# Kernel tuning notes

Measured on AMD Instinct MI355X. Metric: run time of the kernel, lower is better.

Reference implementation:

```python
import jax, jax.numpy as jnp
import numpy as np
import math

D_SINGLE, D_PAIR, H, PQ, PV = 384, 128, 12, 4, 8
DH = D_SINGLE // H
OUT_DIM = H * DH + H * PV * 4 + H * D_PAIR


def setup_inputs() -> dict:
    key = jax.random.key(0)
    ks = jax.random.split(key, 24)
    B, L = 1, 512
    inp = {
        'single': jax.random.normal(ks[0], (B, L, D_SINGLE), jnp.float32),
        'pair': jax.random.normal(ks[1], (B, L, L, D_PAIR), jnp.float32),
        'rot_mats': jax.random.normal(ks[2], (B, L, 3, 3), jnp.float32),
        'trans': jax.random.normal(ks[3], (B, L, 3), jnp.float32),
        'mask': jnp.ones((B, L), jnp.float32),
        'ln_w': jnp.ones((D_SINGLE,), jnp.float32),
        'ln_b': jnp.zeros((D_SINGLE,), jnp.float32),
        'Wq': jax.random.normal(ks[4], (D_SINGLE, H * DH), jnp.float32) * 0.02,
        'bq': jnp.zeros((H * DH,), jnp.float32),
        'Wk': jax.random.normal(ks[5], (D_SINGLE, H * DH), jnp.float32) * 0.02,
        'bk': jnp.zeros((H * DH,), jnp.float32),
        'Wv': jax.random.normal(ks[6], (D_SINGLE, H * DH), jnp.float32) * 0.02,
        'bv': jnp.zeros((H * DH,), jnp.float32),
        'Wqp': jax.random.normal(ks[7], (D_SINGLE, H * PQ * 3), jnp.float32) * 0.02,
        'bqp': jnp.zeros((H * PQ * 3,), jnp.float32),
        'Wkp': jax.random.normal(ks[8], (D_SINGLE, H * PQ * 3), jnp.float32) * 0.02,
        'bkp': jnp.zeros((H * PQ * 3,), jnp.float32),
        'Wvp': jax.random.normal(ks[9], (D_SINGLE, H * PV * 3), jnp.float32) * 0.02,
        'bvp': jnp.zeros((H * PV * 3,), jnp.float32),
        'Wpb': jax.random.normal(ks[10], (D_PAIR, H), jnp.float32) * 0.02,
        'bpb': jnp.zeros((H,), jnp.float32),
        'Wo': jax.random.normal(ks[11], (OUT_DIM, D_SINGLE), jnp.float32) * 0.02,
        'bo': jnp.zeros((D_SINGLE,), jnp.float32),
        'w_c': jnp.asarray(1.0 / math.sqrt(3.0), jnp.float32),
        'w_l': jnp.asarray(1.0 / 3.0, jnp.float32),
        'gamma_h': jnp.ones((H,), jnp.float32),
    }
    return inp


def _layer_norm(x, w, b, eps=1e-5):
    mu = jnp.mean(x, axis=-1, keepdims=True)
    var = jnp.mean((x - mu) ** 2, axis=-1, keepdims=True)
    return (x - mu) * jax.lax.rsqrt(var + eps) * w + b


def reference(single, pair, rot_mats, trans, mask, ln_w, ln_b, Wq, bq, Wk, bk, Wv, bv,
              Wqp, bqp, Wkp, bkp, Wvp, bvp, Wpb, bpb, Wo, bo, w_c, w_l, gamma_h):
    B, L, _ = single.shape
    sn = _layer_norm(single, ln_w, ln_b)
    q = (sn @ Wq + bq).reshape(B, L, H, DH)
    k = (sn @ Wk + bk).reshape(B, L, H, DH)
    v = (sn @ Wv + bv).reshape(B, L, H, DH)
    qp = (sn @ Wqp + bqp).reshape(B, L, H, PQ, 3)
    kp = (sn @ Wkp + bkp).reshape(B, L, H, PQ, 3)
    vp = (sn @ Wvp + bvp).reshape(B, L, H, PV, 3)

    t = trans[:, :, None, None, :]  # [B,L,1,1,3]
    qg = jnp.einsum('blij,blhpj->blhpi', rot_mats, qp) + t
    kg = jnp.einsum('blij,blhpj->blhpi', rot_mats, kp) + t
    vg = jnp.einsum('blij,blhpj->blhpi', rot_mats, vp) + t

    # sequence logits [B,H,L,L]
    seq_logits = jnp.einsum('bihd,bjhd->bhij', q, k) * w_c / math.sqrt(DH)

    # geometric logits: pairwise point distances [B,H,L,L]
    q_pts = jnp.transpose(qg, (0, 2, 1, 3, 4))  # [B,H,L,PQ,3]
    k_pts = jnp.transpose(kg, (0, 2, 1, 3, 4))
    diff = q_pts[:, :, :, None] - k_pts[:, :, None]  # [B,H,L,L,PQ,3]
    dist_sq = jnp.sum(diff ** 2, axis=-1)            # [B,H,L,L,PQ]
    geo_logits = -0.5 * jnp.sum(dist_sq, axis=-1) * gamma_h[None, :, None, None] * w_l

    pair_bias = jnp.transpose(pair @ Wpb + bpb, (0, 3, 1, 2))  # [B,H,L,L]
    logits = seq_logits + geo_logits + pair_bias

    mask_2d = (mask[:, :, None] * mask[:, None, :])[:, None]  # [B,1,L,L]
    logits = jnp.where(mask_2d > 0, logits, jnp.float32(-1e9))
    attn = jax.nn.softmax(logits, axis=-1)  # [B,H,L,L]

    # sequence aggregation -> [B,L,H,DH]
    seq_out = jnp.einsum('bhij,bjhd->bihd', attn, v).reshape(B, L, H * DH)

    # point aggregation -> local frame features
    pts_out = jnp.einsum('bhij,bjhpd->bihpd', attn, vg)  # [B,L,H,PV,3]
    pts_local = jnp.einsum('blji,blhpj->blhpi', rot_mats, pts_out - t)
    pts_norm = jnp.linalg.norm(pts_local, axis=-1, keepdims=True)
    pts_feat = jnp.concatenate([pts_norm, pts_local], axis=-1).reshape(B, L, H * PV * 4)

    # pair aggregation -> [B,L,H*D_PAIR]
    pair_out = jnp.einsum('bhij,bijd->bihd', attn, pair).reshape(B, L, H * D_PAIR)

    combined = jnp.concatenate([seq_out, pts_feat, pair_out], axis=-1)
    return combined @ Wo + bo
```

## Files before the change

### kernel.cpp

```cpp
#include <hip/hip_runtime.h>
#include <math.h>

#define LQ    512
#define DS    384
#define DPAIR 128
#define NH    12
#define NPP   1792
#define FE    48
#define TJC   64
#define NC    8

typedef unsigned short u16;
typedef unsigned int   u32;
typedef __attribute__((ext_vector_type(8))) short bf16x8;
typedef __attribute__((ext_vector_type(4))) float f32x4;

__device__ inline u16 bf16_rne(float x) {
  u32 u = __float_as_uint(x);
  u32 r = (u + 0x7FFFu + ((u >> 16) & 1u)) >> 16;
  return (u16)r;
}
__device__ inline void split_bf16(float x, u16& h, u16& l) {
  u16 hb = bf16_rne(x);
  float hf = __uint_as_float(((u32)hb) << 16);
  h = hb;
  l = bf16_rne(x - hf);
}

__global__ __launch_bounds__(256) void k_concat_wT(
    const float* __restrict__ Wq, const float* __restrict__ Wk,
    const float* __restrict__ Wv, const float* __restrict__ Wqp,
    const float* __restrict__ Wkp, const float* __restrict__ Wvp,
    const float* __restrict__ bq, const float* __restrict__ bk,
    const float* __restrict__ bv, const float* __restrict__ bqp,
    const float* __restrict__ bkp, const float* __restrict__ bvp,
    const float* __restrict__ Wpb,
    u16* __restrict__ Wth, u16* __restrict__ Wtl,
    float* __restrict__ bcat, float* __restrict__ WpbT) {
  int blk = blockIdx.x, t = threadIdx.x;
  if (blk < 168) {
    __shared__ u16 hi[64][66], lo[64][66];
    int kb = blk / 28, cb = blk % 28;
    int k0 = kb * 64, c0 = cb * 64;
    for (int e = t; e < 4096; e += 256) {
      int rr = e >> 6, cc = e & 63;
      int k = k0 + rr, c = c0 + cc;
      float v = 0.f;
      if (c < 384)       v = Wq[k*384 + c];
      else if (c < 768)  v = Wk[k*384 + c-384];
      else if (c < 1152) v = Wv[k*384 + c-768];
      else if (c < 1296) v = Wqp[k*144 + c-1152];
      else if (c < 1440) v = Wkp[k*144 + c-1296];
      else if (c < 1728) v = Wvp[k*288 + c-1440];
      u16 h_, l_; split_bf16(v, h_, l_);
      hi[rr][cc] = h_; lo[rr][cc] = l_;
    }
    __syncthreads();
    for (int e = t; e < 4096; e += 256) {
      int cc = e >> 6, kk = e & 63;
      Wth[(size_t)(c0+cc)*DS + k0 + kk] = hi[kk][cc];
      Wtl[(size_t)(c0+cc)*DS + k0 + kk] = lo[kk][cc];
    }
  } else {
    for (int e = t; e < NPP + NH*DPAIR; e += 256) {
      if (e < NPP) {
        int c = e;
        float v = 0.f;
        if (c < 384)       v = bq[c];
        else if (c < 768)  v = bk[c-384];
        else if (c < 1152) v = bv[c-768];
        else if (c < 1296) v = bqp[c-1152];
        else if (c < 1440) v = bkp[c-1296];
        else if (c < 1728) v = bvp[c-1440];
        bcat[c] = v;
      } else {
        int e2 = e - NPP;
        int k = e2 / NH, h = e2 % NH;
        WpbT[h*DPAIR + k] = Wpb[e2];
      }
    }
  }
}

__global__ __launch_bounds__(256) void k_transpose_split(
    const float* __restrict__ src, u16* __restrict__ dh, u16* __restrict__ dl,
    int R, int Cc) {
  __shared__ u16 hi[64][66], lo[64][66];
  int r0 = blockIdx.x * 64, c0 = blockIdx.y * 64, t = threadIdx.x;
  for (int e = t; e < 4096; e += 256) {
    int rr = e >> 6, cc = e & 63;
    float v = src[(size_t)(r0+rr)*Cc + c0 + cc];
    u16 h_, l_; split_bf16(v, h_, l_);
    hi[rr][cc] = h_; lo[rr][cc] = l_;
  }
  __syncthreads();
  for (int e = t; e < 4096; e += 256) {
    int cc = e >> 6, rr = e & 63;
    dh[(size_t)(c0+cc)*R + r0 + rr] = hi[rr][cc];
    dl[(size_t)(c0+cc)*R + r0 + rr] = lo[rr][cc];
  }
}

__global__ void k_split4(const float* __restrict__ src, u16* __restrict__ h,
                         u16* __restrict__ l, int n4) {
  int e = blockIdx.x * 256 + threadIdx.x;
  if (e >= n4) return;
  float4 v = ((const float4*)src)[e];
  u16 h0,l0,h1,l1,h2,l2,h3,l3;
  split_bf16(v.x, h0, l0); split_bf16(v.y, h1, l1);
  split_bf16(v.z, h2, l2); split_bf16(v.w, h3, l3);
  uint2 hp, lp;
  hp.x = (u32)h0 | ((u32)h1 << 16); hp.y = (u32)h2 | ((u32)h3 << 16);
  lp.x = (u32)l0 | ((u32)l1 << 16); lp.y = (u32)l2 | ((u32)l3 << 16);
  ((uint2*)h)[e] = hp; ((uint2*)l)[e] = lp;
}

__global__ __launch_bounds__(128) void k_layernorm(const float* __restrict__ x,
                                                   const float* __restrict__ w,
                                                   const float* __restrict__ b,
                                                   u16* __restrict__ yh,
                                                   u16* __restrict__ yl) {
  __shared__ float red[128];
  __shared__ float s_mu, s_rstd;
  int i = blockIdx.x, t = threadIdx.x;
  float v0 = x[i*DS + t], v1 = x[i*DS + t + 128], v2 = x[i*DS + t + 256];
  red[t] = v0 + v1 + v2; __syncthreads();
  for (int s = 64; s > 0; s >>= 1) { if (t < s) red[t] += red[t+s]; __syncthreads(); }
  if (t == 0) s_mu = red[0] * (1.f/384.f);
  __syncthreads();
  float mu = s_mu;
  float d0 = v0-mu, d1 = v1-mu, d2 = v2-mu;
  red[t] = d0*d0 + d1*d1 + d2*d2; __syncthreads();
  for (int s = 64; s > 0; s >>= 1) { if (t < s) red[t] += red[t+s]; __syncthreads(); }
  if (t == 0) s_rstd = rsqrtf(red[0] * (1.f/384.f) + 1e-5f);
  __syncthreads();
  float r = s_rstd;
  float y0 = d0*r*w[t      ] + b[t      ];
  float y1 = d1*r*w[t + 128] + b[t + 128];
  float y2 = d2*r*w[t + 256] + b[t + 256];
  u16 h_, l_;
  split_bf16(y0, h_, l_); yh[i*DS + t      ] = h_; yl[i*DS + t      ] = l_;
  split_bf16(y1, h_, l_); yh[i*DS + t + 128] = h_; yl[i*DS + t + 128] = l_;
  split_bf16(y2, h_, l_); yh[i*DS + t + 256] = h_; yl[i*DS + t + 256] = l_;
}

__global__ __launch_bounds__(256) void k_gemm_mfma(
    const u16* __restrict__ Ah, const u16* __restrict__ Al,
    const u16* __restrict__ Bth, const u16* __restrict__ Btl,
    const float* __restrict__ bias, float* __restrict__ C,
    float* __restrict__ Cpart, int M, int N, int K) {
  int t = threadIdx.x;
  int lane = t & 63, wave = t >> 6;
  int wr = wave >> 1, wc = wave & 1;
  int i0 = blockIdx.y * 64 + wr * 32;
  int j0 = blockIdx.x * 64 + wc * 32;
  int KS = gridDim.z;
  int kper = K / KS;
  size_t kbeg = (size_t)blockIdx.z * kper;
  int lr = lane & 15, lk = (lane >> 4) << 3;

  const u16* a0h = Ah  + (size_t)(i0 + lr) * K + kbeg + lk;
  const u16* a1h = a0h + (size_t)16 * K;
  const u16* a0l = Al  + (size_t)(i0 + lr) * K + kbeg + lk;
  const u16* a1l = a0l + (size_t)16 * K;
  const u16* b0h = Bth + (size_t)(j0 + lr) * K + kbeg + lk;
  const u16* b1h = b0h + (size_t)16 * K;
  const u16* b0l = Btl + (size_t)(j0 + lr) * K + kbeg + lk;
  const u16* b1l = b0l + (size_t)16 * K;

  f32x4 c00 = {0.f,0.f,0.f,0.f}, c01 = c00, c10 = c00, c11 = c00;
  for (int k = 0; k < kper; k += 32) {
    bf16x8 A0h = *(const bf16x8*)(a0h + k);
    bf16x8 A1h = *(const bf16x8*)(a1h + k);
    bf16x8 B0h = *(const bf16x8*)(b0h + k);
    bf16x8 B1h = *(const bf16x8*)(b1h + k);
    bf16x8 A0l = *(const bf16x8*)(a0l + k);
    bf16x8 A1l = *(const bf16x8*)(a1l + k);
    bf16x8 B0l = *(const bf16x8*)(b0l + k);
    bf16x8 B1l = *(const bf16x8*)(b1l + k);
    c00 = __builtin_amdgcn_mfma_f32_16x16x32_bf16(A0h, B0h, c00, 0, 0, 0);
    c01 = __builtin_amdgcn_mfma_f32_16x16x32_bf16(A0h, B1h, c01, 0, 0, 0);
    c10 = __builtin_amdgcn_mfma_f32_16x16x32_bf16(A1h, B0h, c10, 0, 0, 0);
    c11 = __builtin_amdgcn_mfma_f32_16x16x32_bf16(A1h, B1h, c11, 0, 0, 0);
    c00 = __builtin_amdgcn_mfma_f32_16x16x32_bf16(A0h, B0l, c00, 0, 0, 0);
    c01 = __builtin_amdgcn_mfma_f32_16x16x32_bf16(A0h, B1l, c01, 0, 0, 0);
    c10 = __builtin_amdgcn_mfma_f32_16x16x32_bf16(A1h, B0l, c10, 0, 0, 0);
    c11 = __builtin_amdgcn_mfma_f32_16x16x32_bf16(A1h, B1l, c11, 0, 0, 0);
    c00 = __builtin_amdgcn_mfma_f32_16x16x32_bf16(A0l, B0h, c00, 0, 0, 0);
    c01 = __builtin_amdgcn_mfma_f32_16x16x32_bf16(A0l, B1h, c01, 0, 0, 0);
    c10 = __builtin_amdgcn_mfma_f32_16x16x32_bf16(A1l, B0h, c10, 0, 0, 0);
    c11 = __builtin_amdgcn_mfma_f32_16x16x32_bf16(A1l, B1h, c11, 0, 0, 0);
  }

  int orow = (lane >> 4) << 2;
  int col0 = j0 + lr, col1 = j0 + 16 + lr;
  if (KS == 1) {
    float bb0 = bias[col0], bb1 = bias[col1];
    #pragma unroll
    for (int r = 0; r < 4; r++) {
      int row0 = i0 + orow + r, row1 = row0 + 16;
      C[(size_t)row0*N + col0] = c00[r] + bb0;
      C[(size_t)row0*N + col1] = c01[r] + bb1;
      C[(size_t)row1*N + col0] = c10[r] + bb0;
      C[(size_t)row1*N + col1] = c11[r] + bb1;
    }
  } else {
    float* dst = Cpart + (size_t)blockIdx.z * M * N;
    #pragma unroll
    for (int r = 0; r < 4; r++) {
      int row0 = i0 + orow + r, row1 = row0 + 16;
      dst[(size_t)row0*N + col0] = c00[r];
      dst[(size_t)row0*N + col1] = c01[r];
      dst[(size_t)row1*N + col0] = c10[r];
      dst[(size_t)row1*N + col1] = c11[r];
    }
  }
}

__global__ void k_reduce_bias(const float* __restrict__ part, const float* __restrict__ bias,
                              float* __restrict__ out, int MN, int N, int KS) {
  int e = blockIdx.x * 256 + threadIdx.x;
  if (e >= MN) return;
  float s = bias[e % N];
  for (int z = 0; z < KS; z++) s += part[(size_t)z*MN + e];
  out[e] = s;
}

__global__ void k_rotfeat(const float* __restrict__ C1, const float* __restrict__ rot,
                          const float* __restrict__ trans, const float* __restrict__ gamma,
                          const float* __restrict__ w_c, const float* __restrict__ w_l,
                          float* __restrict__ Af, float* __restrict__ Bf,
                          float* __restrict__ vgb) {
  int idx = blockIdx.x * 256 + threadIdx.x;
  if (idx >= LQ*NH) return;
  int h = idx % NH, i = idx / NH;
  float R[9], tr[3];
  #pragma unroll
  for (int r = 0; r < 9; r++) R[r] = rot[(size_t)i*9 + r];
  #pragma unroll
  for (int r = 0; r < 3; r++) tr[r] = trans[(size_t)i*3 + r];

  float s  = w_c[0] * rsqrtf(32.f);
  float gp = gamma[h] * w_l[0];
  float* a  = Af + ((size_t)h*LQ + i)*FE;
  float* bb = Bf + ((size_t)h*LQ + i)*FE;
  const float* q = C1 + (size_t)i*NPP + h*32;
  const float* k = C1 + (size_t)i*NPP + 384 + h*32;
  #pragma unroll 8
  for (int d = 0; d < 32; d++) { a[d] = s*q[d]; bb[d] = k[d]; }

  const float* qp = C1 + (size_t)i*NPP + 1152 + h*12;
  const float* kp = C1 + (size_t)i*NPP + 1296 + h*12;
  float sq = 0.f, sk = 0.f;
  #pragma unroll
  for (int p = 0; p < 4; p++) {
    float x = qp[p*3], y = qp[p*3+1], z = qp[p*3+2];
    #pragma unroll
    for (int r = 0; r < 3; r++) {
      float g = fmaf(R[r*3],x, fmaf(R[r*3+1],y, fmaf(R[r*3+2],z, tr[r])));
      a[32 + p*3 + r] = gp*g;
      sq = fmaf(g,g,sq);
    }
    float xk = kp[p*3], yk = kp[p*3+1], zk = kp[p*3+2];
    #pragma unroll
    for (int r = 0; r < 3; r++) {
      float g = fmaf(R[r*3],xk, fmaf(R[r*3+1],yk, fmaf(R[r*3+2],zk, tr[r])));
      bb[32 + p*3 + r] = g;
      sk = fmaf(g,g,sk);
    }
  }
  a[44] = -0.5f*gp*sq; a[45] = 1.f; a[46] = 0.f; a[47] = 0.f;
  bb[44] = 1.f; bb[45] = -0.5f*gp*sk; bb[46] = 0.f; bb[47] = 0.f;

  const float* vp = C1 + (size_t)i*NPP + 1440 + h*24;
  float* vd = vgb + ((size_t)i*NH + h)*24;
  #pragma unroll
  for (int p = 0; p < 8; p++) {
    float x = vp[p*3], y = vp[p*3+1], z = vp[p*3+2];
    #pragma unroll
    for (int r = 0; r < 3; r++)
      vd[p*3 + r] = fmaf(R[r*3],x, fmaf(R[r*3+1],y, fmaf(R[r*3+2],z, tr[r])));
  }
}

__global__ __launch_bounds__(256) void k_logits_nt(const float* __restrict__ Af,
                                                   const float* __restrict__ Bf,
                                                   float* __restrict__ S) {
  __shared__ float As[48*68];
  __shared__ float Bs[48*68];
  int h = blockIdx.z;
  int i0 = blockIdx.y * 64, j0 = blockIdx.x * 64;
  int t = threadIdx.x;
  int mg = t >> 4, ng = t & 15;
  const float* Ahp = Af + (size_t)h*LQ*FE;
  const float* Bhp = Bf + (size_t)h*LQ*FE;
  for (int e = t; e < 64*48; e += 256) {
    int m = e / 48, k = e % 48;
    As[k*68 + m] = Ahp[(size_t)(i0+m)*FE + k];
    Bs[k*68 + m] = Bhp[(size_t)(j0+m)*FE + k];
  }
  __syncthreads();
  float acc[4][4] = {};
  #pragma unroll 8
  for (int k = 0; k < 48; k++) {
    float4 av = *(const float4*)(As + k*68 + mg*4);
    float4 bv = *(const float4*)(Bs + k*68 + ng*4);
    float a[4] = {av.x, av.y, av.z, av.w};
    float b[4] = {bv.x, bv.y, bv.z, bv.w};
    #pragma unroll
    for (int y = 0; y < 4; y++)
      #pragma unroll
      for (int x = 0; x < 4; x++)
        acc[y][x] = fmaf(a[y], b[x], acc[y][x]);
  }
  #pragma unroll
  for (int y = 0; y < 4; y++) {
    #pragma unroll
    for (int x = 0; x < 4; x++)
      S[((size_t)h*LQ + i0 + mg*4 + y)*LQ + j0 + ng*4 + x] = acc[y][x];
  }
}

__global__ __launch_bounds__(256, 2) void k_pair_chunk(
    const float* __restrict__ pair, const float* __restrict__ WpbT,
    const float* __restrict__ bpb, const float* __restrict__ mask,
    float* __restrict__ S, float* __restrict__ pairpart, float* __restrict__ msum) {
  __shared__ float tile[TJC*133];
  __shared__ float wt[NH*TJC];
  int i = blockIdx.x, c = blockIdx.y, t = threadIdx.x;
  int j0 = c*TJC;

  const float4* src = (const float4*)(pair + ((size_t)i*LQ + j0)*DPAIR);
  #pragma unroll
  for (int u = 0; u < 8; u++) {
    int e = t + u*256; int row = e >> 5, c4 = e & 31;
    *(float4*)&tile[row*133 + c4*4] = src[e];
  }

  int j = t & 63;
  int hg = __builtin_amdgcn_readfirstlane(t >> 6);
  int h0 = hg*3;
  float l[3];
  #pragma unroll
  for (int q = 0; q < 3; q++)
    l[q] = S[((size_t)(h0+q)*LQ + i)*LQ + j0 + j] + bpb[h0+q];
  bool dead = (mask[i] * mask[j0 + j] <= 0.f);
  __syncthreads();

  {
    const float* w0p = WpbT + (size_t)(h0+0)*DPAIR;
    const float* w1p = WpbT + (size_t)(h0+1)*DPAIR;
    const float* w2p = WpbT + (size_t)(h0+2)*DPAIR;
    float a0 = 0.f, a1 = 0.f, a2 = 0.f;
    #pragma unroll 8
    for (int k = 0; k < DPAIR; k += 4) {
      float4 pv = *(const float4*)&tile[j*133 + k];
      float4 w0 = *(const float4*)(w0p + k);
      float4 w1 = *(const float4*)(w1p + k);
      float4 w2 = *(const float4*)(w2p + k);
      a0 = fmaf(pv.x,w0.x, fmaf(pv.y,w0.y, fmaf(pv.z,w0.z, fmaf(pv.w,w0.w, a0))));
      a1 = fmaf(pv.x,w1.x, fmaf(pv.y,w1.y, fmaf(pv.z,w1.z, fmaf(pv.w,w1.w, a1))));
      a2 = fmaf(pv.x,w2.x, fmaf(pv.y,w2.y, fmaf(pv.z,w2.z, fmaf(pv.w,w2.w, a2))));
    }
    l[0] += a0; l[1] += a1; l[2] += a2;
    if (dead) { l[0] = -1e9f; l[1] = -1e9f; l[2] = -1e9f; }
  }

  #pragma unroll
  for (int q = 0; q < 3; q++) {
    float m = l[q];
    #pragma unroll
    for (int o = 32; o > 0; o >>= 1) m = fmaxf(m, __shfl_xor(m, o, 64));
// ... 14 lines not shown
  float4 pv[8];
  #pragma unroll
  for (int q = 0; q < 8; q++) pv[q] = *(const float4*)&tile[(jb+q)*133 + dg*4];
  float4 acc[NH];
  #pragma unroll
  for (int h = 0; h < NH; h++) acc[h] = make_float4(0.f,0.f,0.f,0.f);
  #pragma unroll
  for (int h = 0; h < NH; h++) {
    float4 w0 = *(const float4*)&wt[h*TJC + jb];
    float4 w1 = *(const float4*)&wt[h*TJC + jb + 4];
    float wq[8] = {w0.x,w0.y,w0.z,w0.w,w1.x,w1.y,w1.z,w1.w};
    float4 a = acc[h];
    #pragma unroll
    for (int q = 0; q < 8; q++) {
      a.x = fmaf(wq[q], pv[q].x, a.x);
      a.y = fmaf(wq[q], pv[q].y, a.y);
      a.z = fmaf(wq[q], pv[q].z, a.z);
      a.w = fmaf(wq[q], pv[q].w, a.w);
    }
    acc[h] = a;
  }
  __syncthreads();

  float4* red4 = (float4*)tile;
  float4 tot[2];
  tot[0] = make_float4(0.f,0.f,0.f,0.f);
  tot[1] = make_float4(0.f,0.f,0.f,0.f);
  #pragma unroll
  for (int half = 0; half < 2; half++) {
    if ((strip >> 2) == half) {
      #pragma unroll
      for (int h = 0; h < NH; h++)
        red4[(((strip & 3)*NH) + h)*32 + dg] = acc[h];
    }
    __syncthreads();
    for (int e = t, u = 0; e < NH*32; e += 256, u++) {
      int rh = e >> 5, rd = e & 31;
      #pragma unroll
      for (int s4 = 0; s4 < 4; s4++) {
        float4 v = red4[((s4*NH) + rh)*32 + rd];
        tot[u].x += v.x; tot[u].y += v.y; tot[u].z += v.z; tot[u].w += v.w;
      }
    }
    __syncthreads();
  }
  for (int e = t, u = 0; e < NH*32; e += 256, u++) {
    int rh = e >> 5, rd = e & 31;
    *(float4*)&pairpart[(((size_t)i*NC + c)*NH + rh)*DPAIR + rd*4] = tot[u];
  }
}

__global__ __launch_bounds__(384) void k_scs_pairout(
    const float* __restrict__ msum, const float* __restrict__ pairpart,
    float* __restrict__ scs_g, float* __restrict__ comb) {
  __shared__ float scs[NH*NC];
  int i = blockIdx.x, t = threadIdx.x;
  if (t < NH) {
    float m = -3.0e38f;
    float mc[NC], sc_[NC];
    #pragma unroll
    for (int c = 0; c < NC; c++) {
      const float* p = msum + (((size_t)i*NC + c)*NH + t)*2;
      mc[c] = p[0]; sc_[c] = p[1];
      m = fmaxf(m, mc[c]);
    }
    float s = 0.f;
    #pragma unroll
    for (int c = 0; c < NC; c++) s += sc_[c] * __expf(mc[c] - m);
    float inv = 1.f / s;
    #pragma unroll
    for (int c = 0; c < NC; c++) {
      float v = __expf(mc[c] - m) * inv;
      scs[t*NC + c] = v;
      scs_g[((size_t)i*NH + t)*NC + c] = v;
    }
  }
  __syncthreads();
  int h = t >> 5, d = t & 31;
  float4 tot = make_float4(0.f,0.f,0.f,0.f);
  #pragma unroll
  for (int c = 0; c < NC; c++) {
    float sc = scs[h*NC + c];
    float4 v = *(const float4*)&pairpart[(((size_t)i*NC + c)*NH + h)*DPAIR + d*4];
    tot.x = fmaf(v.x, sc, tot.x); tot.y = fmaf(v.y, sc, tot.y);
    tot.z = fmaf(v.z, sc, tot.z); tot.w = fmaf(v.w, sc, tot.w);
  }
  *(float4*)&comb[(size_t)i*2304 + 768 + h*DPAIR + d*4] = tot;
}

__global__ __launch_bounds__(256) void k_attn_v(const float* __restrict__ attn,
                                                const float* __restrict__ C1,
                                                const float* __restrict__ vg,
                                                const float* __restrict__ scs,
                                                float* __restrict__ psum) {
  __shared__ float As[64*68];
  __shared__ float Vs[64*68];
  int i0 = blockIdx.x * 64;
  int h = blockIdx.y;
  int z = blockIdx.z;
  int t = threadIdx.x;
  int mg = t >> 4, ng = t & 15;
  float acc[4][4] = {};
  for (int k0 = z*128; k0 < z*128 + 128; k0 += 64) {
    int c = k0 >> 6;
    __syncthreads();
    for (int e = t; e < 64*64; e += 256) {
      int m = e >> 6, j = e & 63;
      float sc = scs[((size_t)(i0+m)*NH + h)*NC + c];
      As[j*68 + m] = attn[((size_t)h*LQ + i0 + m)*LQ + k0 + j] * sc;
    }
    for (int e = t; e < 64*64; e += 256) {
      int j = e >> 6, cc = e & 63;
      float v = 0.f;
      if (cc < 32)      v = C1[(size_t)(k0+j)*NPP + 768 + h*32 + cc];
      else if (cc < 56) v = vg[((size_t)(k0+j)*NH + h)*24 + (cc-32)];
      Vs[j*68 + cc] = v;
    }
    __syncthreads();
    #pragma unroll 4
    for (int j = 0; j < 64; j++) {
      float4 av = *(const float4*)(As + j*68 + mg*4);
      float4 bv = *(const float4*)(Vs + j*68 + ng*4);
      float a[4] = {av.x, av.y, av.z, av.w};
      float b[4] = {bv.x, bv.y, bv.z, bv.w};
      #pragma unroll
      for (int y = 0; y < 4; y++)
        #pragma unroll
        for (int x = 0; x < 4; x++)
          acc[y][x] = fmaf(a[y], b[x], acc[y][x]);
    }
  }
  #pragma unroll
  for (int y = 0; y < 4; y++) {
    int i = i0 + mg*4 + y;
    #pragma unroll
    for (int x = 0; x < 4; x++) {
      int n = ng*4 + x;
      psum[(((size_t)z*LQ + i)*NH + h)*64 + n] = acc[y][x];
    }
  }
}

__global__ void k_avpts(const float* __restrict__ psum, const float* __restrict__ rot,
                        const float* __restrict__ trans, float* __restrict__ comb) {
  int idx = blockIdx.x * 256 + threadIdx.x;
  if (idx >= LQ*NH*40) return;
  int w = idx % 40; int ih = idx / 40; int h = ih % NH; int i = ih / NH;
  size_t base = ((size_t)i*NH + h)*64;
  if (w < 32) {
    float s = 0.f;
    for (int z = 0; z < 4; z++) s += psum[(size_t)z*LQ*NH*64 + base + w];
    comb[(size_t)i*2304 + h*32 + w] = s;
  } else {
    int p = w - 32;
    float g[3];
    #pragma unroll
    for (int r = 0; r < 3; r++) {
      int n = 32 + p*3 + r;
      float s = 0.f;
      for (int z = 0; z < 4; z++) s += psum[(size_t)z*LQ*NH*64 + base + n];
      g[r] = s;
    }
    const float* R = rot + (size_t)i*9;
    const float* tr = trans + (size_t)i*3;
    float x = g[0]-tr[0], y = g[1]-tr[1], z = g[2]-tr[2];
    float lx = fmaf(R[0],x, fmaf(R[3],y, R[6]*z));
    float ly = fmaf(R[1],x, fmaf(R[4],y, R[7]*z));
    float lz = fmaf(R[2],x, fmaf(R[5],y, R[8]*z));
    float nrm = sqrtf(fmaf(lx,lx, fmaf(ly,ly, lz*lz)));
    float* dst = comb + (size_t)i*2304 + 384 + (h*8 + p)*4;
    dst[0] = nrm; dst[1] = lx; dst[2] = ly; dst[3] = lz;
  }
}

extern "C" void kernel_launch(void* const* d_in, const int* in_sizes, int n_in,
                              void* d_out, int out_size, void* d_ws, size_t ws_size,
                              hipStream_t stream) {
  const float* single = (const float*)d_in[0];
  const float* pair   = (const float*)d_in[1];
  const float* rot    = (const float*)d_in[2];
  const float* trans  = (const float*)d_in[3];
  const float* mask   = (const float*)d_in[4];
  const float* ln_w   = (const float*)d_in[5];
  const float* ln_b   = (const float*)d_in[6];
  const float* Wq     = (const float*)d_in[7];
  const float* bq     = (const float*)d_in[8];
  const float* Wk     = (const float*)d_in[9];
  const float* bk     = (const float*)d_in[10];
  const float* Wv     = (const float*)d_in[11];
  const float* bv     = (const float*)d_in[12];
  const float* Wqp    = (const float*)d_in[13];
  const float* bqp    = (const float*)d_in[14];
  const float* Wkp    = (const float*)d_in[15];
  const float* bkp    = (const float*)d_in[16];
  const float* Wvp    = (const float*)d_in[17];
  const float* bvp    = (const float*)d_in[18];
  const float* Wpb    = (const float*)d_in[19];
  const float* bpb    = (const float*)d_in[20];
  const float* Wo     = (const float*)d_in[21];
  const float* bo     = (const float*)d_in[22];
  const float* w_c    = (const float*)d_in[23];
  const float* w_l    = (const float*)d_in[24];
  const float* gamma  = (const float*)d_in[25];
  float* out = (float*)d_out;

  float* p = (float*)d_ws;
  auto alloc = [&](size_t n) { float* r = p; p += n; return r; };
  u16* WcatTh = (u16*)alloc((size_t)NPP*DS/2);
  u16* WcatTl = (u16*)alloc((size_t)NPP*DS/2);
  u16* snh    = (u16*)alloc((size_t)LQ*DS/2);
  u16* snl    = (u16*)alloc((size_t)LQ*DS/2);
  u16* WoTh   = (u16*)alloc((size_t)DS*2304/2);
  u16* WoTl   = (u16*)alloc((size_t)DS*2304/2);
  u16* combh  = (u16*)alloc((size_t)LQ*2304/2);
  u16* combl  = (u16*)alloc((size_t)LQ*2304/2);
  float* bcat    = alloc(NPP);
  float* WpbT    = alloc((size_t)NH*DPAIR);
  float* C1      = alloc((size_t)LQ*NPP);
  float* vgb     = alloc((size_t)LQ*NH*24);
  float* Af      = alloc((size_t)NH*LQ*FE);
  float* Bf      = alloc((size_t)NH*LQ*FE);
  float* S       = alloc((size_t)NH*LQ*LQ);
  float* pairpart= alloc((size_t)LQ*NC*NH*DPAIR);
  float* msum    = alloc((size_t)LQ*NC*NH*2);
  float* scs_g   = alloc((size_t)LQ*NH*NC);
  float* comb    = alloc((size_t)LQ*2304);
  float* scratch = alloc((size_t)2*LQ*NPP);

  k_concat_wT<<<dim3(169), 256, 0, stream>>>(
      Wq, Wk, Wv, Wqp, Wkp, Wvp, bq, bk, bv, bqp, bkp, bvp, Wpb,
      WcatTh, WcatTl, bcat, WpbT);
  k_transpose_split<<<dim3(2304/64, DS/64), 256, 0, stream>>>(Wo, WoTh, WoTl, 2304, DS);
  k_layernorm<<<dim3(LQ), 128, 0, stream>>>(single, ln_w, ln_b, snh, snl);
  k_gemm_mfma<<<dim3(NPP/64, LQ/64, 1), 256, 0, stream>>>(
      snh, snl, WcatTh, WcatTl, bcat, C1, nullptr, LQ, NPP, DS);
  k_rotfeat<<<dim3((LQ*NH + 255)/256), 256, 0, stream>>>(C1, rot, trans, gamma, w_c, w_l, Af, Bf, vgb);
  k_logits_nt<<<dim3(LQ/64, LQ/64, NH), 256, 0, stream>>>(Af, Bf, S);
  k_pair_chunk<<<dim3(LQ, NC), 256, 0, stream>>>(pair, WpbT, bpb, mask, S, pairpart, msum);
  k_scs_pairout<<<dim3(LQ), 384, 0, stream>>>(msum, pairpart, scs_g, comb);
  k_attn_v<<<dim3(LQ/64, NH, 4), 256, 0, stream>>>(S, C1, vgb, scs_g, scratch);
  k_avpts<<<dim3((LQ*NH*40 + 255)/256), 256, 0, stream>>>(scratch, rot, trans, comb);
  k_split4<<<dim3((LQ*2304/4 + 255)/256), 256, 0, stream>>>(comb, combh, combl, LQ*2304/4);
  k_gemm_mfma<<<dim3(DS/64, LQ/64, 8), 256, 0, stream>>>(
      combh, combl, WoTh, WoTl, nullptr, nullptr, scratch, LQ, DS, 2304);
  k_reduce_bias<<<dim3((LQ*DS + 255)/256), 256, 0, stream>>>(scratch, bo, out, LQ*DS, DS, 8);
}
```

Baseline: 384.2 us.

## Move logits and attention-value GEMMs to split-bf16 MFMA and fuse prep kernels

Replaces the scalar FP32 logits and attention-times-values GEMMs with split-bf16 MFMA kernels (hi/lo, three products), padding features to 64. The producers (rotfeat, scs_pairout, avpts) now emit bf16 hi/lo operands directly. This removes the separate split4 pass and the fp32 comb buffer. The weight-transpose, Wo-transpose and layernorm kernels are merged into one launch. In exchange it adds an extra pass that writes the scaled attention weights as two bf16 arrays, and rounding error from the split-bf16 approximation.

```diff
diff --git a/kernel.cpp b/kernel.cpp
--- a/kernel.cpp
+++ b/kernel.cpp
@@ -6,7 +6,7 @@
 #define DPAIR 128
 #define NH    12
 #define NPP   1792
-#define FE    48
+#define FE2   64
 #define TJC   64
 #define NC    8
 
@@ -27,19 +27,23 @@
   l = bf16_rne(x - hf);
 }
 
-__global__ __launch_bounds__(256) void k_concat_wT(
+__global__ __launch_bounds__(256) void k_prep(
     const float* __restrict__ Wq, const float* __restrict__ Wk,
     const float* __restrict__ Wv, const float* __restrict__ Wqp,
     const float* __restrict__ Wkp, const float* __restrict__ Wvp,
     const float* __restrict__ bq, const float* __restrict__ bk,
     const float* __restrict__ bv, const float* __restrict__ bqp,
     const float* __restrict__ bkp, const float* __restrict__ bvp,
-    const float* __restrict__ Wpb,
+    const float* __restrict__ Wpb, const float* __restrict__ Wo,
+    const float* __restrict__ xs, const float* __restrict__ ln_w,
+    const float* __restrict__ ln_b,
     u16* __restrict__ Wth, u16* __restrict__ Wtl,
-    float* __restrict__ bcat, float* __restrict__ WpbT) {
+    float* __restrict__ bcat, float* __restrict__ WpbT,
+    u16* __restrict__ WoTh, u16* __restrict__ WoTl,
+    u16* __restrict__ snh, u16* __restrict__ snl) {
+  __shared__ u16 sh_hi[64][66], sh_lo[64][66];
   int blk = blockIdx.x, t = threadIdx.x;
   if (blk < 168) {
-    __shared__ u16 hi[64][66], lo[64][66];
     int kb = blk / 28, cb = blk % 28;
     int k0 = kb * 64, c0 = cb * 64;
     for (int e = t; e < 4096; e += 256) {
@@ -53,15 +57,15 @@
       else if (c < 1440) v = Wkp[k*144 + c-1296];
       else if (c < 1728) v = Wvp[k*288 + c-1440];
       u16 h_, l_; split_bf16(v, h_, l_);
-      hi[rr][cc] = h_; lo[rr][cc] = l_;
+      sh_hi[rr][cc] = h_; sh_lo[rr][cc] = l_;
     }
     __syncthreads();
     for (int e = t; e < 4096; e += 256) {
       int cc = e >> 6, kk = e & 63;
-      Wth[(size_t)(c0+cc)*DS + k0 + kk] = hi[kk][cc];
-      Wtl[(size_t)(c0+cc)*DS + k0 + kk] = lo[kk][cc];
-    }
-  } else {
+      Wth[(size_t)(c0+cc)*DS + k0 + kk] = sh_hi[kk][cc];
+      Wtl[(size_t)(c0+cc)*DS + k0 + kk] = sh_lo[kk][cc];
+    }
+  } else if (blk == 168) {
     for (int e = t; e < NPP + NH*DPAIR; e += 256) {
       if (e < NPP) {
         int c = e;
@@ -79,69 +83,43 @@
         WpbT[h*DPAIR + k] = Wpb[e2];
       }
     }
-  }
-}
-
-__global__ __launch_bounds__(256) void k_transpose_split(
-    const float* __restrict__ src, u16* __restrict__ dh, u16* __restrict__ dl,
-    int R, int Cc) {
-  __shared__ u16 hi[64][66], lo[64][66];
-  int r0 = blockIdx.x * 64, c0 = blockIdx.y * 64, t = threadIdx.x;
-  for (int e = t; e < 4096; e += 256) {
-    int rr = e >> 6, cc = e & 63;
-    float v = src[(size_t)(r0+rr)*Cc + c0 + cc];
-    u16 h_, l_; split_bf16(v, h_, l_);
-    hi[rr][cc] = h_; lo[rr][cc] = l_;
-  }
-  __syncthreads();
-  for (int e = t; e < 4096; e += 256) {
-    int cc = e >> 6, rr = e & 63;
-    dh[(size_t)(c0+cc)*R + r0 + rr] = hi[rr][cc];
-    dl[(size_t)(c0+cc)*R + r0 + rr] = lo[rr][cc];
-  }
-}
-
-__global__ void k_split4(const float* __restrict__ src, u16* __restrict__ h,
-                         u16* __restrict__ l, int n4) {
-  int e = blockIdx.x * 256 + threadIdx.x;
-  if (e >= n4) return;
-  float4 v = ((const float4*)src)[e];
-  u16 h0,l0,h1,l1,h2,l2,h3,l3;
-  split_bf16(v.x, h0, l0); split_bf16(v.y, h1, l1);
-  split_bf16(v.z, h2, l2); split_bf16(v.w, h3, l3);
-  uint2 hp, lp;
-  hp.x = (u32)h0 | ((u32)h1 << 16); hp.y = (u32)h2 | ((u32)h3 << 16);
-  lp.x = (u32)l0 | ((u32)l1 << 16); lp.y = (u32)l2 | ((u32)l3 << 16);
-  ((uint2*)h)[e] = hp; ((uint2*)l)[e] = lp;
-}
-
-__global__ __launch_bounds__(128) void k_layernorm(const float* __restrict__ x,
-                                                   const float* __restrict__ w,
-                                                   const float* __restrict__ b,
-                                                   u16* __restrict__ yh,
-                                                   u16* __restrict__ yl) {
-  __shared__ float red[128];
-  __shared__ float s_mu, s_rstd;
-  int i = blockIdx.x, t = threadIdx.x;
-  float v0 = x[i*DS + t], v1 = x[i*DS + t + 128], v2 = x[i*DS + t + 256];
-  red[t] = v0 + v1 + v2; __syncthreads();
-  for (int s = 64; s > 0; s >>= 1) { if (t < s) red[t] += red[t+s]; __syncthreads(); }
-  if (t == 0) s_mu = red[0] * (1.f/384.f);
-  __syncthreads();
-  float mu = s_mu;
-  float d0 = v0-mu, d1 = v1-mu, d2 = v2-mu;
-  red[t] = d0*d0 + d1*d1 + d2*d2; __syncthreads();
-  for (int s = 64; s > 0; s >>= 1) { if (t < s) red[t] += red[t+s]; __syncthreads(); }
-  if (t == 0) s_rstd = rsqrtf(red[0] * (1.f/384.f) + 1e-5f);
-  __syncthreads();
-  float r = s_rstd;
-  float y0 = d0*r*w[t      ] + b[t      ];
-  float y1 = d1*r*w[t + 128] + b[t + 128];
-  float y2 = d2*r*w[t + 256] + b[t + 256];
-  u16 h_, l_;
-  split_bf16(y0, h_, l_); yh[i*DS + t      ] = h_; yl[i*DS + t      ] = l_;
-  split_bf16(y1, h_, l_); yh[i*DS + t + 128] = h_; yl[i*DS + t + 128] = l_;
-  split_bf16(y2, h_, l_); yh[i*DS + t + 256] = h_; yl[i*DS + t + 256] = l_;
+  } else if (blk < 385) {
+    int idx = blk - 169;
+    int kt = idx % 36, nt = idx / 36;
+    int k0 = kt * 64, n0 = nt * 64;
+    for (int e = t; e < 4096; e += 256) {
+      int rr = e >> 6, cc = e & 63;
+      float v = Wo[(size_t)(k0+rr)*384 + n0 + cc];
+      u16 h_, l_; split_bf16(v, h_, l_);
+      sh_hi[rr][cc] = h_; sh_lo[rr][cc] = l_;
+    }
+    __syncthreads();
+    for (int e = t; e < 4096; e += 256) {
+      int cc = e >> 6, kk = e & 63;
+      WoTh[(size_t)(n0+cc)*2304 + k0 + kk] = sh_hi[kk][cc];
+      WoTl[(size_t)(n0+cc)*2304 + k0 + kk] = sh_lo[kk][cc];
+    }
+  } else {
+    int i = blk - 385;
+    float* red = (float*)&sh_hi[0][0];
+    float a0 = xs[i*DS + t];
+    float a1 = (t < 128) ? xs[i*DS + 256 + t] : 0.f;
+    red[t] = a0 + a1; __syncthreads();
+    for (int s = 128; s > 0; s >>= 1) { if (t < s) red[t] += red[t+s]; __syncthreads(); }
+    float mu = red[0] * (1.f/384.f);
+    __syncthreads();
+    float d0 = a0 - mu, d1 = (t < 128) ? (a1 - mu) : 0.f;
+    red[t] = d0*d0 + d1*d1; __syncthreads();
+    for (int s = 128; s > 0; s >>= 1) { if (t < s) red[t] += red[t+s]; __syncthreads(); }
+    float rstd = rsqrtf(red[0] * (1.f/384.f) + 1e-5f);
+    u16 h_, l_;
+    float y0 = d0*rstd*ln_w[t] + ln_b[t];
+    split_bf16(y0, h_, l_); snh[i*DS + t] = h_; snl[i*DS + t] = l_;
+    if (t < 128) {
+      float y1 = d1*rstd*ln_w[256+t] + ln_b[256+t];
+      split_bf16(y1, h_, l_); snh[i*DS + 256 + t] = h_; snl[i*DS + 256 + t] = l_;
+    }
+  }
 }
 
 __global__ __launch_bounds__(256) void k_gemm_mfma(
@@ -229,8 +207,9 @@
 __global__ void k_rotfeat(const float* __restrict__ C1, const float* __restrict__ rot,
                           const float* __restrict__ trans, const float* __restrict__ gamma,
                           const float* __restrict__ w_c, const float* __restrict__ w_l,
-                          float* __restrict__ Af, float* __restrict__ Bf,
-                          float* __restrict__ vgb) {
+                          u16* __restrict__ Afh, u16* __restrict__ Afl,
+                          u16* __restrict__ Bfh, u16* __restrict__ Bfl,
+                          u16* __restrict__ Vth, u16* __restrict__ Vtl) {
   int idx = blockIdx.x * 256 + threadIdx.x;
   if (idx >= LQ*NH) return;
   int h = idx % NH, i = idx / NH;
@@ -242,12 +221,15 @@
 
   float s  = w_c[0] * rsqrtf(32.f);
   float gp = gamma[h] * w_l[0];
-  float* a  = Af + ((size_t)h*LQ + i)*FE;
-  float* bb = Bf + ((size_t)h*LQ + i)*FE;
+  size_t ab = ((size_t)h*LQ + i)*FE2;
   const float* q = C1 + (size_t)i*NPP + h*32;
   const float* k = C1 + (size_t)i*NPP + 384 + h*32;
+  u16 h_, l_;
   #pragma unroll 8
-  for (int d = 0; d < 32; d++) { a[d] = s*q[d]; bb[d] = k[d]; }
+  for (int d = 0; d < 32; d++) {
+    split_bf16(s*q[d], h_, l_); Afh[ab+d] = h_; Afl[ab+d] = l_;
+    split_bf16(k[d],   h_, l_); Bfh[ab+d] = h_; Bfl[ab+d] = l_;
+  }
 
   const float* qp = C1 + (size_t)i*NPP + 1152 + h*12;
   const float* kp = C1 + (size_t)i*NPP + 1296 + h*12;
@@ -258,66 +240,104 @@
     #pragma unroll
     for (int r = 0; r < 3; r++) {
       float g = fmaf(R[r*3],x, fmaf(R[r*3+1],y, fmaf(R[r*3+2],z, tr[r])));
-      a[32 + p*3 + r] = gp*g;
+      split_bf16(gp*g, h_, l_); Afh[ab+32+p*3+r] = h_; Afl[ab+32+p*3+r] = l_;
       sq = fmaf(g,g,sq);
     }
     float xk = kp[p*3], yk = kp[p*3+1], zk = kp[p*3+2];
     #pragma unroll
     for (int r = 0; r < 3; r++) {
       float g = fmaf(R[r*3],xk, fmaf(R[r*3+1],yk, fmaf(R[r*3+2],zk, tr[r])));
-      bb[32 + p*3 + r] = g;
+      split_bf16(g, h_, l_); Bfh[ab+32+p*3+r] = h_; Bfl[ab+32+p*3+r] = l_;
       sk = fmaf(g,g,sk);
     }
   }
-  a[44] = -0.5f*gp*sq; a[45] = 1.f; a[46] = 0.f; a[47] = 0.f;
-  bb[44] = 1.f; bb[45] = -0.5f*gp*sk; bb[46] = 0.f; bb[47] = 0.f;
+  split_bf16(-0.5f*gp*sq, h_, l_); Afh[ab+44] = h_; Afl[ab+44] = l_;
+  split_bf16(1.f, h_, l_);         Afh[ab+45] = h_; Afl[ab+45] = l_;
+  split_bf16(1.f, h_, l_);         Bfh[ab+44] = h_; Bfl[ab+44] = l_;
+  split_bf16(-0.5f*gp*sk, h_, l_); Bfh[ab+45] = h_; Bfl[ab+45] = l_;
+  #pragma unroll
+  for (int d = 46; d < FE2; d++) {
+    Afh[ab+d] = 0; Afl[ab+d] = 0; Bfh[ab+d] = 0; Bfl[ab+d] = 0;
+  }
 
   const float* vp = C1 + (size_t)i*NPP + 1440 + h*24;
-  float* vd = vgb + ((size_t)i*NH + h)*24;
+  #pragma unroll 8
+  for (int n = 0; n < 32; n++) {
+    split_bf16(C1[(size_t)i*NPP + 768 + h*32 + n], h_, l_);
+    Vth[((size_t)h*64 + n)*LQ + i] = h_; Vtl[((size_t)h*64 + n)*LQ + i] = l_;
+  }
   #pragma unroll
   for (int p = 0; p < 8; p++) {
     float x = vp[p*3], y = vp[p*3+1], z = vp[p*3+2];
     #pragma unroll
-    for (int r = 0; r < 3; r++)
-      vd[p*3 + r] = fmaf(R[r*3],x, fmaf(R[r*3+1],y, fmaf(R[r*3+2],z, tr[r])));
-  }
-}
-
-__global__ __launch_bounds__(256) void k_logits_nt(const float* __restrict__ Af,
-                                                   const float* __restrict__ Bf,
-                                                   float* __restrict__ S) {
-  __shared__ float As[48*68];
-  __shared__ float Bs[48*68];
+    for (int r = 0; r < 3; r++) {
+      float g = fmaf(R[r*3],x, fmaf(R[r*3+1],y, fmaf(R[r*3+2],z, tr[r])));
+      split_bf16(g, h_, l_);
+      Vth[((size_t)h*64 + 32 + p*3 + r)*LQ + i] = h_;
+      Vtl[((size_t)h*64 + 32 + p*3 + r)*LQ + i] = l_;
+    }
+  }
+  #pragma unroll
+  for (int n = 56; n < 64; n++) {
+    Vth[((size_t)h*64 + n)*LQ + i] = 0; Vtl[((size_t)h*64 + n)*LQ + i] = 0;
+  }
+}
+
+__global__ __launch_bounds__(256) void k_logits_mfma(
+    const u16* __restrict__ Afh, const u16* __restrict__ Afl,
+    const u16* __restrict__ Bfh, const u16* __restrict__ Bfl,
+    float* __restrict__ S) {
+  int t = threadIdx.x;
+  int lane = t & 63, wave = t >> 6;
+  int wr = wave >> 1, wc = wave & 1;
   int h = blockIdx.z;
-  int i0 = blockIdx.y * 64, j0 = blockIdx.x * 64;
-  int t = threadIdx.x;
-  int mg = t >> 4, ng = t & 15;
-  const float* Ahp = Af + (size_t)h*LQ*FE;
-  const float* Bhp = Bf + (size_t)h*LQ*FE;
-  for (int e = t; e < 64*48; e += 256) {
-    int m = e / 48, k = e % 48;
-    As[k*68 + m] = Ahp[(size_t)(i0+m)*FE + k];
-    Bs[k*68 + m] = Bhp[(size_t)(j0+m)*FE + k];
-  }
-  __syncthreads();
-  float acc[4][4] = {};
-  #pragma unroll 8
-  for (int k = 0; k < 48; k++) {
-    float4 av = *(const float4*)(As + k*68 + mg*4);
-    float4 bv = *(const float4*)(Bs + k*68 + ng*4);
-    float a[4] = {av.x, av.y, av.z, av.w};
-    float b[4] = {bv.x, bv.y, bv.z, bv.w};
-    #pragma unroll
-    for (int y = 0; y < 4; y++)
-      #pragma unroll
-      for (int x = 0; x < 4; x++)
-        acc[y][x] = fmaf(a[y], b[x], acc[y][x]);
-  }
-  #pragma unroll
-  for (int y = 0; y < 4; y++) {
-    #pragma unroll
-    for (int x = 0; x < 4; x++)
-      S[((size_t)h*LQ + i0 + mg*4 + y)*LQ + j0 + ng*4 + x] = acc[y][x];
+  int i0 = blockIdx.y * 64 + wr * 32;
+  int j0 = blockIdx.x * 64 + wc * 32;
+  int lr = lane & 15, lk = (lane >> 4) << 3;
+
+  const u16* a0h = Afh + ((size_t)h*LQ + i0 + lr)*FE2 + lk;
+  const u16* a1h = a0h + (size_t)16*FE2;
+  const u16* a0l = Afl + ((size_t)h*LQ + i0 + lr)*FE2 + lk;
+  const u16* a1l = a0l + (size_t)16*FE2;
+  const u16* b0h = Bfh + ((size_t)h*LQ + j0 + lr)*FE2 + lk;
+  const u16* b1h = b0h + (size_t)16*FE2;
+  const u16* b0l = Bfl + ((size_t)h*LQ + j0 + lr)*FE2 + lk;
+  const u16* b1l = b0l + (size_t)16*FE2;
+
+  f32x4 c00 = {0.f,0.f,0.f,0.f}, c01 = c00, c10 = c00, c11 = c00;
+  #pragma unroll
+  for (int k = 0; k < FE2; k += 32) {
+    bf16x8 A0h = *(const bf16x8*)(a0h + k);
+    bf16x8 A1h = *(const bf16x8*)(a1h + k);
+    bf16x8 B0h = *(const bf16x8*)(b0h + k);
+    bf16x8 B1h = *(const bf16x8*)(b1h + k);
+    bf16x8 A0l = *(const bf16x8*)(a0l + k);
+    bf16x8 A1l = *(const bf16x8*)(a1l + k);
+    bf16x8 B0l = *(const bf16x8*)(b0l + k);
+    bf16x8 B1l = *(const bf16x8*)(b1l + k);
+    c00 = __builtin_amdgcn_mfma_f32_16x16x32_bf16(A0h, B0h, c00, 0, 0, 0);
+    c01 = __builtin_amdgcn_mfma_f32_16x16x32_bf16(A0h, B1h, c01, 0, 0, 0);
+    c10 = __builtin_amdgcn_mfma_f32_16x16x32_bf16(A1h, B0h, c10, 0, 0, 0);
+    c11 = __builtin_amdgcn_mfma_f32_16x16x32_bf16(A1h, B1h, c11, 0, 0, 0);
+    c00 = __builtin_amdgcn_mfma_f32_16x16x32_bf16(A0h, B0l, c00, 0, 0, 0);
+    c01 = __builtin_amdgcn_mfma_f32_16x16x32_bf16(A0h, B1l, c01, 0, 0, 0);
+    c10 = __builtin_amdgcn_mfma_f32_16x16x32_bf16(A1h, B0l, c10, 0, 0, 0);
+    c11 = __builtin_amdgcn_mfma_f32_16x16x32_bf16(A1h, B1l, c11, 0, 0, 0);
+    c00 = __builtin_amdgcn_mfma_f32_16x16x32_bf16(A0l, B0h, c00, 0, 0, 0);
+    c01 = __builtin_amdgcn_mfma_f32_16x16x32_bf16(A0l, B1h, c01, 0, 0, 0);
+    c10 = __builtin_amdgcn_mfma_f32_16x16x32_bf16(A1l, B0h, c10, 0, 0, 0);
+    c11 = __builtin_amdgcn_mfma_f32_16x16x32_bf16(A1l, B1h, c11, 0, 0, 0);
+  }
+
+  int orow = (lane >> 4) << 2;
+  int col0 = j0 + lr, col1 = j0 + 16 + lr;
+  #pragma unroll
+  for (int r = 0; r < 4; r++) {
+    int row0 = i0 + orow + r, row1 = row0 + 16;
+    S[((size_t)h*LQ + row0)*LQ + col0] = c00[r];
+    S[((size_t)h*LQ + row0)*LQ + col1] = c01[r];
+    S[((size_t)h*LQ + row1)*LQ + col0] = c10[r];
+    S[((size_t)h*LQ + row1)*LQ + col1] = c11[r];
   }
 }
 
@@ -438,7 +458,9 @@
 
 __global__ __launch_bounds__(384) void k_scs_pairout(
     const float* __restrict__ msum, const float* __restrict__ pairpart,
-    float* __restrict__ scs_g, float* __restrict__ comb) {
+    const float* __restrict__ S,
+    u16* __restrict__ Awh, u16* __restrict__ Awl,
+    u16* __restrict__ combh, u16* __restrict__ combl) {
   __shared__ float scs[NH*NC];
   int i = blockIdx.x, t = threadIdx.x;
   if (t < NH) {
@@ -455,11 +477,8 @@
     for (int c = 0; c < NC; c++) s += sc_[c] * __expf(mc[c] - m);
     float inv = 1.f / s;
     #pragma unroll
-    for (int c = 0; c < NC; c++) {
-      float v = __expf(mc[c] - m) * inv;
-      scs[t*NC + c] = v;
-      scs_g[((size_t)i*NH + t)*NC + c] = v;
-    }
+    for (int c = 0; c < NC; c++)
+      scs[t*NC + c] = __expf(mc[c] - m) * inv;
   }
   __syncthreads();
   int h = t >> 5, d = t & 31;
@@ -471,72 +490,95 @@
     tot.x = fmaf(v.x, sc, tot.x); tot.y = fmaf(v.y, sc, tot.y);
     tot.z = fmaf(v.z, sc, tot.z); tot.w = fmaf(v.w, sc, tot.w);
   }
-  *(float4*)&comb[(size_t)i*2304 + 768 + h*DPAIR + d*4] = tot;
-}
-
-__global__ __launch_bounds__(256) void k_attn_v(const float* __restrict__ attn,
-                                                const float* __restrict__ C1,
-                                                const float* __restrict__ vg,
-                                                const float* __restrict__ scs,
-                                                float* __restrict__ psum) {
-  __shared__ float As[64*68];
-  __shared__ float Vs[64*68];
-  int i0 = blockIdx.x * 64;
-  int h = blockIdx.y;
-  int z = blockIdx.z;
+  size_t cb = (size_t)i*2304 + 768 + h*DPAIR + d*4;
+  u16 h_, l_;
+  split_bf16(tot.x, h_, l_); combh[cb+0] = h_; combl[cb+0] = l_;
+  split_bf16(tot.y, h_, l_); combh[cb+1] = h_; combl[cb+1] = l_;
+  split_bf16(tot.z, h_, l_); combh[cb+2] = h_; combl[cb+2] = l_;
+  split_bf16(tot.w, h_, l_); combh[cb+3] = h_; combl[cb+3] = l_;
+  for (int e = t; e < NH*LQ; e += 384) {
+    int hh2 = e >> 9, j = e & 511;
+    float w = S[((size_t)hh2*LQ + i)*LQ + j] * scs[hh2*NC + (j >> 6)];
+    split_bf16(w, h_, l_);
+    Awh[((size_t)hh2*LQ + i)*LQ + j] = h_;
+    Awl[((size_t)hh2*LQ + i)*LQ + j] = l_;
+  }
+}
+
+__global__ __launch_bounds__(256) void k_attn_mfma(
+    const u16* __restrict__ Awh, const u16* __restrict__ Awl,
+    const u16* __restrict__ Vth, const u16* __restrict__ Vtl,
+    float* __restrict__ psum) {
   int t = threadIdx.x;
-  int mg = t >> 4, ng = t & 15;
-  float acc[4][4] = {};
-  for (int k0 = z*128; k0 < z*128 + 128; k0 += 64) {
-    int c = k0 >> 6;
-    __syncthreads();
-    for (int e = t; e < 64*64; e += 256) {
-      int m = e >> 6, j = e & 63;
-      float sc = scs[((size_t)(i0+m)*NH + h)*NC + c];
-      As[j*68 + m] = attn[((size_t)h*LQ + i0 + m)*LQ + k0 + j] * sc;
-    }
-    for (int e = t; e < 64*64; e += 256) {
-      int j = e >> 6, cc = e & 63;
-      float v = 0.f;
-      if (cc < 32)      v = C1[(size_t)(k0+j)*NPP + 768 + h*32 + cc];
-      else if (cc < 56) v = vg[((size_t)(k0+j)*NH + h)*24 + (cc-32)];
-      Vs[j*68 + cc] = v;
-    }
-    __syncthreads();
-    #pragma unroll 4
-    for (int j = 0; j < 64; j++) {
-      float4 av = *(const float4*)(As + j*68 + mg*4);
-      float4 bv = *(const float4*)(Vs + j*68 + ng*4);
-      float a[4] = {av.x, av.y, av.z, av.w};
-      float b[4] = {bv.x, bv.y, bv.z, bv.w};
-      #pragma unroll
-      for (int y = 0; y < 4; y++)
-        #pragma unroll
-        for (int x = 0; x < 4; x++)
-          acc[y][x] = fmaf(a[y], b[x], acc[y][x]);
-    }
-  }
-  #pragma unroll
-  for (int y = 0; y < 4; y++) {
-    int i = i0 + mg*4 + y;
-    #pragma unroll
-    for (int x = 0; x < 4; x++) {
-      int n = ng*4 + x;
-      psum[(((size_t)z*LQ + i)*NH + h)*64 + n] = acc[y][x];
-    }
+  int lane = t & 63, wave = t >> 6;
+  int wr = wave >> 1, wc = wave & 1;
+  int z = blockIdx.x;
+  int i0 = blockIdx.y * 64 + wr * 32;
+  int h = blockIdx.z;
+  int n0 = wc * 32;
+  int lr = lane & 15, lk = (lane >> 4) << 3;
+  size_t kb = (size_t)z*128 + lk;
+
+  const u16* a0h = Awh + ((size_t)h*LQ + i0 + lr)*LQ + kb;
+  const u16* a1h = a0h + (size_t)16*LQ;
+  const u16* a0l = Awl + ((size_t)h*LQ + i0 + lr)*LQ + kb;
+  const u16* a1l = a0l + (size_t)16*LQ;
+  const u16* b0h = Vth + ((size_t)h*64 + n0 + lr)*LQ + kb;
+  const u16* b1h = b0h + (size_t)16*LQ;
+  const u16* b0l = Vtl + ((size_t)h*64 + n0 + lr)*LQ + kb;
+  const u16* b1l = b0l + (size_t)16*LQ;
+
+  f32x4 c00 = {0.f,0.f,0.f,0.f}, c01 = c00, c10 = c00, c11 = c00;
+  #pragma unroll
+  for (int k = 0; k < 128; k += 32) {
+    bf16x8 A0h = *(const bf16x8*)(a0h + k);
+    bf16x8 A1h = *(const bf16x8*)(a1h + k);
+    bf16x8 B0h = *(const bf16x8*)(b0h + k);
+    bf16x8 B1h = *(const bf16x8*)(b1h + k);
+    bf16x8 A0l = *(const bf16x8*)(a0l + k);
+    bf16x8 A1l = *(const bf16x8*)(a1l + k);
+    bf16x8 B0l = *(const bf16x8*)(b0l + k);
+    bf16x8 B1l = *(const bf16x8*)(b1l + k);
+    c00 = __builtin_amdgcn_mfma_f32_16x16x32_bf16(A0h, B0h, c00, 0, 0, 0);
+    c01 = __builtin_amdgcn_mfma_f32_16x16x32_bf16(A0h, B1h, c01, 0, 0, 0);
+    c10 = __builtin_amdgcn_mfma_f32_16x16x32_bf16(A1h, B0h, c10, 0, 0, 0);
+    c11 = __builtin_amdgcn_mfma_f32_16x16x32_bf16(A1h, B1h, c11, 0, 0, 0);
+    c00 = __builtin_amdgcn_mfma_f32_16x16x32_bf16(A0h, B0l, c00, 0, 0, 0);
+    c01 = __builtin_amdgcn_mfma_f32_16x16x32_bf16(A0h, B1l, c01, 0, 0, 0);
+    c10 = __builtin_amdgcn_mfma_f32_16x16x32_bf16(A1h, B0l, c10, 0, 0, 0);
+    c11 = __builtin_amdgcn_mfma_f32_16x16x32_bf16(A1h, B1l, c11, 0, 0, 0);
+    c00 = __builtin_amdgcn_mfma_f32_16x16x32_bf16(A0l, B0h, c00, 0, 0, 0);
+    c01 = __builtin_amdgcn_mfma_f32_16x16x32_bf16(A0l, B1h, c01, 0, 0, 0);
+    c10 = __builtin_amdgcn_mfma_f32_16x16x32_bf16(A1l, B0h, c10, 0, 0, 0);
+    c11 = __builtin_amdgcn_mfma_f32_16x16x32_bf16(A1l, B1h, c11, 0, 0, 0);
+  }
+
+  int orow = (lane >> 4) << 2;
+  int col0 = n0 + lr, col1 = n0 + 16 + lr;
+  #pragma unroll
+  for (int r = 0; r < 4; r++) {
+    int row0 = i0 + orow + r, row1 = row0 + 16;
+    psum[(((size_t)z*LQ + row0)*NH + h)*64 + col0] = c00[r];
+    psum[(((size_t)z*LQ + row0)*NH + h)*64 + col1] = c01[r];
+    psum[(((size_t)z*LQ + row1)*NH + h)*64 + col0] = c10[r];
+    psum[(((size_t)z*LQ + row1)*NH + h)*64 + col1] = c11[r];
   }
 }
 
 __global__ void k_avpts(const float* __restrict__ psum, const float* __restrict__ rot,
-                        const float* __restrict__ trans, float* __restrict__ comb) {
+                        const float* __restrict__ trans,
+                        u16* __restrict__ combh, u16* __restrict__ combl) {
   int idx = blockIdx.x * 256 + threadIdx.x;
   if (idx >= LQ*NH*40) return;
   int w = idx % 40; int ih = idx / 40; int h = ih % NH; int i = ih / NH;
   size_t base = ((size_t)i*NH + h)*64;
+  u16 h_, l_;
   if (w < 32) {
     float s = 0.f;
     for (int z = 0; z < 4; z++) s += psum[(size_t)z*LQ*NH*64 + base + w];
-    comb[(size_t)i*2304 + h*32 + w] = s;
+    split_bf16(s, h_, l_);
+    combh[(size_t)i*2304 + h*32 + w] = h_;
+    combl[(size_t)i*2304 + h*32 + w] = l_;
   } else {
     int p = w - 32;
     float g[3];
@@ -554,8 +596,11 @@
     float ly = fmaf(R[1],x, fmaf(R[4],y, R[7]*z));
     float lz = fmaf(R[2],x, fmaf(R[5],y, R[8]*z));
     float nrm = sqrtf(fmaf(lx,lx, fmaf(ly,ly, lz*lz)));
-    float* dst = comb + (size_t)i*2304 + 384 + (h*8 + p)*4;
-    dst[0] = nrm; dst[1] = lx; dst[2] = ly; dst[3] = lz;
+    size_t dst = (size_t)i*2304 + 384 + (h*8 + p)*4;
+    split_bf16(nrm, h_, l_); combh[dst+0] = h_; combl[dst+0] = l_;
+    split_bf16(lx,  h_, l_); combh[dst+1] = h_; combl[dst+1] = l_;
+    split_bf16(ly,  h_, l_); combh[dst+2] = h_; combl[dst+2] = l_;
+    split_bf16(lz,  h_, l_); combh[dst+3] = h_; combl[dst+3] = l_;
   }
 }
 
@@ -600,34 +645,36 @@
   u16* WoTl   = (u16*)alloc((size_t)DS*2304/2);
   u16* combh  = (u16*)alloc((size_t)LQ*2304/2);
   u16* combl  = (u16*)alloc((size_t)LQ*2304/2);
+  u16* Afh    = (u16*)alloc((size_t)NH*LQ*FE2/2);
+  u16* Afl    = (u16*)alloc((size_t)NH*LQ*FE2/2);
+  u16* Bfh    = (u16*)alloc((size_t)NH*LQ*FE2/2);
+  u16* Bfl    = (u16*)alloc((size_t)NH*LQ*FE2/2);
+  u16* Vth    = (u16*)alloc((size_t)NH*64*LQ/2);
+  u16* Vtl    = (u16*)alloc((size_t)NH*64*LQ/2);
+  u16* Awh    = (u16*)alloc((size_t)NH*LQ*LQ/2);
+  u16* Awl    = (u16*)alloc((size_t)NH*LQ*LQ/2);
   float* bcat    = alloc(NPP);
   float* WpbT    = alloc((size_t)NH*DPAIR);
   float* C1      = alloc((size_t)LQ*NPP);
-  float* vgb     = alloc((size_t)LQ*NH*24);
-  float* Af      = alloc((size_t)NH*LQ*FE);
-  float* Bf      = alloc((size_t)NH*LQ*FE);
   float* S       = alloc((size_t)NH*LQ*LQ);
   float* pairpart= alloc((size_t)LQ*NC*NH*DPAIR);
   float* msum    = alloc((size_t)LQ*NC*NH*2);
-  float* scs_g   = alloc((size_t)LQ*NH*NC);
-  float* comb    = alloc((size_t)LQ*2304);
-  float* scratch = alloc((size_t)2*LQ*NPP);
-
-  k_concat_wT<<<dim3(169), 256, 0, stream>>>(
-      Wq, Wk, Wv, Wqp, Wkp, Wvp, bq, bk, bv, bqp, bkp, bvp, Wpb,
-      WcatTh, WcatTl, bcat, WpbT);
-  k_transpose_split<<<dim3(2304/64, DS/64), 256, 0, stream>>>(Wo, WoTh, WoTl, 2304, DS);
-  k_layernorm<<<dim3(LQ), 128, 0, stream>>>(single, ln_w, ln_b, snh, snl);
+  float* psum    = alloc((size_t)4*LQ*NH*64);
+  float* outpart = alloc((size_t)8*LQ*DS);
+
+  k_prep<<<dim3(897), 256, 0, stream>>>(
+      Wq, Wk, Wv, Wqp, Wkp, Wvp, bq, bk, bv, bqp, bkp, bvp, Wpb, Wo,
+      single, ln_w, ln_b, WcatTh, WcatTl, bcat, WpbT, WoTh, WoTl, snh, snl);
   k_gemm_mfma<<<dim3(NPP/64, LQ/64, 1), 256, 0, stream>>>(
       snh, snl, WcatTh, WcatTl, bcat, C1, nullptr, LQ, NPP, DS);
-  k_rotfeat<<<dim3((LQ*NH + 255)/256), 256, 0, stream>>>(C1, rot, trans, gamma, w_c, w_l, Af, Bf, vgb);
-  k_logits_nt<<<dim3(LQ/64, LQ/64, NH), 256, 0, stream>>>(Af, Bf, S);
+  k_rotfeat<<<dim3((LQ*NH + 255)/256), 256, 0, stream>>>(
+      C1, rot, trans, gamma, w_c, w_l, Afh, Afl, Bfh, Bfl, Vth, Vtl);
+  k_logits_mfma<<<dim3(LQ/64, LQ/64, NH), 256, 0, stream>>>(Afh, Afl, Bfh, Bfl, S);
   k_pair_chunk<<<dim3(LQ, NC), 256, 0, stream>>>(pair, WpbT, bpb, mask, S, pairpart, msum);
-  k_scs_pairout<<<dim3(LQ), 384, 0, stream>>>(msum, pairpart, scs_g, comb);
-  k_attn_v<<<dim3(LQ/64, NH, 4), 256, 0, stream>>>(S, C1, vgb, scs_g, scratch);
-  k_avpts<<<dim3((LQ*NH*40 + 255)/256), 256, 0, stream>>>(scratch, rot, trans, comb);
-  k_split4<<<dim3((LQ*2304/4 + 255)/256), 256, 0, stream>>>(comb, combh, combl, LQ*2304/4);
+  k_scs_pairout<<<dim3(LQ), 384, 0, stream>>>(msum, pairpart, S, Awh, Awl, combh, combl);
+  k_attn_mfma<<<dim3(4, LQ/64, NH), 256, 0, stream>>>(Awh, Awl, Vth, Vtl, psum);
+  k_avpts<<<dim3((LQ*NH*40 + 255)/256), 256, 0, stream>>>(psum, rot, trans, combh, combl);
   k_gemm_mfma<<<dim3(DS/64, LQ/64, 8), 256, 0, stream>>>(
-      combh, combl, WoTh, WoTl, nullptr, nullptr, scratch, LQ, DS, 2304);
-  k_reduce_bias<<<dim3((LQ*DS + 255)/256), 256, 0, stream>>>(scratch, bo, out, LQ*DS, DS, 8);
-}
+      combh, combl, WoTh, WoTl, nullptr, nullptr, outpart, LQ, DS, 2304);
+  k_reduce_bias<<<dim3((LQ*DS + 255)/256), 256, 0, stream>>>(outpart, bo, out, LQ*DS, DS, 8);
+}
```

Measured after the change: 366.3 us. 4.7% less time.
